# Kernel optimization log

Measured on AMD Instinct MI355X. Metric: run time of the kernel, lower is better.

The kernel has to match this reference:

```python
import jax, jax.numpy as jnp
import numpy as np

H, L, OUT = 128, 3, 128
N, E, NRG, ERG, M, G = 200_000, 600_000, 100_000, 300_000, 200_000, 10_000
BN_EPS = 1e-5


def setup_inputs() -> dict:
    key = jax.random.key(0)
    ks = iter(jax.random.split(key, 32))
    rint = lambda shape, hi: jax.random.randint(next(ks), shape, 0, hi, dtype=jnp.int64 if False else jnp.int32)
    inp = {
        "node_feat": rint((N, 9), 100),
        "edge_index": rint((2, E), N),
        "edge_feat": rint((E, 3), 100),
        "batch": jnp.sort(rint((N,), G)),
        "mapping_row": rint((M,), N),
        "mapping_col": rint((M,), NRG),
        "rg_edge_index": rint((2, ERG), NRG),
        "rg_atom_features": rint((NRG,), 8),
        "tree_batch": jnp.sort(rint((NRG,), G)),
        "num_graphs": G,
    }
    s = 0.05
    nrm = lambda shape: jax.random.normal(next(ks), shape, dtype=jnp.float32) * s
    inp.update({
        "atom_emb": nrm((9, 100, H)),
        "bond_emb": nrm((L, 3, 100, H)),
        "rg_emb": nrm((8, H)),
        "atom_W1": nrm((L, H, 2 * H)),
        "atom_W2": nrm((L, 2 * H, H)),
        "rg_W1": nrm((L, H, 2 * H)),
        "rg_W2": nrm((L, 2 * H, H)),
        "raw2rg_W": nrm((L, H, H)),
        "rg2raw_W": nrm((L, H, H)),
        "atom_lin_W": nrm((H, H)),
        "rg_lin_W": nrm((H, H)),
        "lin_W": nrm((H, OUT)),
    })
    return inp


def _scatter_mean(src, idx, n):
    s = jax.ops.segment_sum(src, idx, num_segments=n)
    c = jax.ops.segment_sum(jnp.ones((src.shape[0], 1), src.dtype), idx, num_segments=n)
    return s / jnp.maximum(c, 1.0)


def _bn(h):  # BatchNorm1d(affine=False), batch statistics
    mu = h.mean(0)
    var = h.var(0)
    return (h - mu) * jax.lax.rsqrt(var + BN_EPS)


def _gin_mlp(h, W1, W2):  # Linear -> BN -> ReLU -> Linear (all bias-free)
    return jax.nn.relu(_bn(h @ W1)) @ W2


def reference(node_feat, edge_index, edge_feat, batch, mapping_row, mapping_col,
              rg_edge_index, rg_atom_features, tree_batch, num_graphs,
              atom_emb, bond_emb, rg_emb, atom_W1, atom_W2, rg_W1, rg_W2,
              raw2rg_W, rg2raw_W, atom_lin_W, rg_lin_W, lin_W):
    n = node_feat.shape[0]
    n_rg = rg_atom_features.shape[0]
    src, dst = edge_index[0], edge_index[1]
    rsrc, rdst = rg_edge_index[0], rg_edge_index[1]

    # AtomEncoder: sum of 9 embedding lookups -> [n, H]
    x = atom_emb[jnp.arange(9), node_feat].sum(axis=1)
    rg = rg_emb[rg_atom_features]  # [n_rg, H]

    for i in range(L):
        # BondEncoder + GINEConv: sum_j relu(x_j + e_ij) aggregated at dst
        e = bond_emb[i][jnp.arange(3), edge_feat].sum(axis=1)  # [E, H]
        agg = jax.ops.segment_sum(jax.nn.relu(x[src] + e), dst, num_segments=n)
        x = jax.nn.relu(_bn(_gin_mlp(x + agg, atom_W1[i], atom_W2[i])))

        # raw -> reduced-graph inter message passing (scatter mean over mapping)
        rg = rg + jax.nn.relu(_scatter_mean(x[mapping_row], mapping_col, n_rg) @ raw2rg_W[i])

        # GINConv on reduced graph
        agg_rg = jax.ops.segment_sum(rg[rsrc], rdst, num_segments=n_rg)
        rg = jax.nn.relu(_bn(_gin_mlp(rg + agg_rg, rg_W1[i], rg_W2[i])))

        # reduced-graph -> raw inter message passing
        x = x + jax.nn.relu(_scatter_mean(rg[mapping_col], mapping_row, n) @ rg2raw_W[i])

    # graph-level readout (mean pooling)
    xg = _scatter_mean(x, batch, num_graphs) @ atom_lin_W
    rgg = _scatter_mean(rg, tree_batch, num_graphs) @ rg_lin_W
    return jax.nn.relu(xg + rgg) @ lin_W  # [num_graphs, OUT]
```

## Files before the change

### kernel.cpp

```cpp
#include <hip/hip_runtime.h>
#include <hip/hip_bf16.h>
#include <cstdint>
#include <cstddef>

#define H 128

using f32x4v = __attribute__((ext_vector_type(4))) float;
using bf8 = __attribute__((ext_vector_type(8))) short;

__device__ __forceinline__ short f2bf(float f) {
  unsigned u = __float_as_uint(f);
  u = (u + 0x7fffu + ((u >> 16) & 1u)) >> 16;
  return (short)u;
}
__device__ __forceinline__ float bf2f(short h) {
  return __uint_as_float(((unsigned)(unsigned short)h) << 16);
}
__device__ __forceinline__ void splitf(float f, short& h, short& l) {
  h = f2bf(f);
  l = f2bf(f - bf2f(h));
}
__device__ __forceinline__ f32x4v mfma16(bf8 a, bf8 b, f32x4v c) {
  return __builtin_amdgcn_mfma_f32_16x16x32_bf16(a, b, c, 0, 0, 0);
}

__device__ __forceinline__ void stage16(const void* gsrc, void* ldst) {
  __builtin_amdgcn_global_load_lds(
      (const __attribute__((address_space(1))) void*)gsrc,
      (__attribute__((address_space(3))) void*)ldst, 16, 0, 0);
}

__device__ __forceinline__ void load_afrags(const float* __restrict__ Ap, bool av,
    float sc, bf8* ah, bf8* al_) {
#pragma unroll
  for (int ks = 0; ks < 4; ++ks) {
    float v[8];
    if (av) {
      f32x4v p0 = *(const f32x4v*)(Ap + ks * 32);
      f32x4v p1 = *(const f32x4v*)(Ap + ks * 32 + 4);
      v[0]=p0.x*sc; v[1]=p0.y*sc; v[2]=p0.z*sc; v[3]=p0.w*sc;
      v[4]=p1.x*sc; v[5]=p1.y*sc; v[6]=p1.z*sc; v[7]=p1.w*sc;
    } else {
#pragma unroll
      for (int j = 0; j < 8; ++j) v[j] = 0.f;
    }
#pragma unroll
    for (int j = 0; j < 8; ++j) { short hh, ll; splitf(v[j], hh, ll); ah[ks][j]=hh; al_[ks][j]=ll; }
  }
}


__global__ __launch_bounds__(256) void pack_w_k(const float* __restrict__ W,
    short* __restrict__ hi, short* __restrict__ lo, int K, int N) {
  int total = K * N;
  int t = blockIdx.x * 256 + threadIdx.x;
  int layer = blockIdx.y;
  if (t >= total) return;
  int k = t / N, n = t - k * N;
  float f = W[(size_t)layer * total + t];
  short h, l; splitf(f, h, l);
  int nt = n >> 4, ks = k >> 5, kk = k & 31;
  int lane = (n & 15) | (((kk >> 3) & 3) << 4);
  size_t idx = (size_t)layer * total + ((size_t)(nt * (K >> 5) + ks) << 9) + lane * 8 + (kk & 7);
  hi[idx] = h; lo[idx] = l;
}


__global__ __launch_bounds__(256) void atom_encode_k(const int* __restrict__ nf,
    const float* __restrict__ emb, float* __restrict__ x, int N) {
  long long t = (long long)blockIdx.x * 256 + threadIdx.x;
  if (t >= (long long)N * H) return;
  int n = (int)(t >> 7), h = (int)(t & 127);
  const int* row = nf + (size_t)n * 9;
  float s = 0.f;
#pragma unroll
  for (int f = 0; f < 9; ++f) s += emb[((size_t)f * 100 + row[f]) * H + h];
  x[t] = s;
}

__global__ __launch_bounds__(256) void rg_init_k(const int* __restrict__ feat,
    const float* __restrict__ emb, float* __restrict__ rg, int NRG) {
  long long t = (long long)blockIdx.x * 256 + threadIdx.x;
  if (t >= (long long)NRG * H) return;
  int n = (int)(t >> 7), h = (int)(t & 127);
  rg[t] = emb[(size_t)feat[n] * H + h];
}


__global__ __launch_bounds__(256) void icount_k(const int* __restrict__ idx,
    int* __restrict__ cnt, int n) {
  int t = blockIdx.x * 256 + threadIdx.x;
  if (t < n) atomicAdd(&cnt[idx[t]], 1);
}

__global__ __launch_bounds__(256) void inv_from_int_k(const int* __restrict__ c,
    float* __restrict__ inv, int n) {
  int t = blockIdx.x * 256 + threadIdx.x;
  if (t < n) inv[t] = 1.0f / (float)max(c[t], 1);
}

__global__ __launch_bounds__(256) void seg_blocksum_k(const int* __restrict__ cnt,
    int* __restrict__ bsum, int n) {
  __shared__ int red[256];
  int base = blockIdx.x * 1024;
  int s = 0;
  for (int i = threadIdx.x; i < 1024; i += 256) {
    int idx = base + i;
    s += (idx < n) ? cnt[idx] : 0;
  }
  red[threadIdx.x] = s; __syncthreads();
  for (int st = 128; st > 0; st >>= 1) {
    if (threadIdx.x < st) red[threadIdx.x] += red[threadIdx.x + st];
    __syncthreads();
  }
  if (threadIdx.x == 0) bsum[blockIdx.x] = red[0];
}

__global__ __launch_bounds__(256) void seg_scan_k(const int* __restrict__ cnt,
    const int* __restrict__ bsum, int* __restrict__ off, int* __restrict__ cur,
    int n, int nblk) {
  __shared__ int pref;
  __shared__ int tsum[257];
  int b = blockIdx.x;
  if (threadIdx.x == 0) {
    int p = 0;
    for (int j = 0; j < b; ++j) p += bsum[j];
    pref = p;
  }
  int base = b * 1024 + threadIdx.x * 4;
  int v[4]; int s = 0;
#pragma unroll
  for (int j = 0; j < 4; ++j) { int idx = base + j; v[j] = (idx < n) ? cnt[idx] : 0; s += v[j]; }
  tsum[threadIdx.x + 1] = s;
  if (threadIdx.x == 0) tsum[0] = 0;
  __syncthreads();
  if (threadIdx.x == 0) { for (int j = 1; j <= 256; ++j) tsum[j] += tsum[j - 1]; }
  __syncthreads();
  int run = pref + tsum[threadIdx.x];
#pragma unroll
  for (int j = 0; j < 4; ++j) {
    int idx = base + j;
    if (idx < n) { off[idx] = run; cur[idx] = run; }
    run += v[j];
  }
  if (b == 0 && threadIdx.x == 0) {
    int tot = 0;
    for (int j = 0; j < nblk; ++j) tot += bsum[j];
    off[n] = tot;
  }
}

__global__ __launch_bounds__(256) void seg_fill_k(const int* __restrict__ idx,
    int* __restrict__ cur, int* __restrict__ ids, int n) {
  int t = blockIdx.x * 256 + threadIdx.x;
  if (t < n) { int p = atomicAdd(&cur[idx[t]], 1); ids[p] = t; }
}


__global__ __launch_bounds__(256) void gine_agg_k(const int* __restrict__ off,
    const int* __restrict__ ids, const int* __restrict__ ei, const int* __restrict__ ef,
    const float* __restrict__ bemb, const float* __restrict__ x,
    float* __restrict__ out, int N) {
  int n = blockIdx.x * 8 + (threadIdx.x >> 5);
  if (n >= N) return;
  int c4 = (threadIdx.x & 31) * 4;
  float4 acc = *(const float4*)(x + (size_t)n * H + c4);
  float4 acc2 = make_float4(0.f, 0.f, 0.f, 0.f);
  int p0 = off[n], p1 = off[n + 1];
  int p = p0;
  for (; p + 1 < p1; p += 2) {
    int e0 = ids[p], e1 = ids[p + 1];
    int s0 = ei[e0], s1 = ei[e1];
    const int* f0 = ef + (size_t)e0 * 3;
    const int* f1 = ef + (size_t)e1 * 3;
    float4 a0 = *(const float4*)(bemb + (size_t)f0[0] * H + c4);
    float4 a1 = *(const float4*)(bemb + ((size_t)100 + f0[1]) * H + c4);
    float4 a2 = *(const float4*)(bemb + ((size_t)200 + f0[2]) * H + c4);
    float4 xa = *(const float4*)(x + (size_t)s0 * H + c4);
    float4 b0 = *(const float4*)(bemb + (size_t)f1[0] * H + c4);
    float4 b1 = *(const float4*)(bemb + ((size_t)100 + f1[1]) * H + c4);
    float4 b2 = *(const float4*)(bemb + ((size_t)200 + f1[2]) * H + c4);
    float4 xb = *(const float4*)(x + (size_t)s1 * H + c4);
    acc.x += fmaxf(xa.x + a0.x + a1.x + a2.x, 0.f);
    acc.y += fmaxf(xa.y + a0.y + a1.y + a2.y, 0.f);
    acc.z += fmaxf(xa.z + a0.z + a1.z + a2.z, 0.f);
    acc.w += fmaxf(xa.w + a0.w + a1.w + a2.w, 0.f);
    acc2.x += fmaxf(xb.x + b0.x + b1.x + b2.x, 0.f);
    acc2.y += fmaxf(xb.y + b0.y + b1.y + b2.y, 0.f);
    acc2.z += fmaxf(xb.z + b0.z + b1.z + b2.z, 0.f);
    acc2.w += fmaxf(xb.w + b0.w + b1.w + b2.w, 0.f);
  }
  if (p < p1) {
    int e = ids[p];
    int src = ei[e];
    const int* f = ef + (size_t)e * 3;
    float4 v0 = *(const float4*)(bemb + (size_t)f[0] * H + c4);
    float4 v1 = *(const float4*)(bemb + ((size_t)100 + f[1]) * H + c4);
    float4 v2 = *(const float4*)(bemb + ((size_t)200 + f[2]) * H + c4);
    float4 xs = *(const float4*)(x + (size_t)src * H + c4);
    acc.x += fmaxf(xs.x + v0.x + v1.x + v2.x, 0.f);
    acc.y += fmaxf(xs.y + v0.y + v1.y + v2.y, 0.f);
    acc.z += fmaxf(xs.z + v0.z + v1.z + v2.z, 0.f);
    acc.w += fmaxf(xs.w + v0.w + v1.w + v2.w, 0.f);
  }
  acc.x += acc2.x; acc.y += acc2.y; acc.z += acc2.z; acc.w += acc2.w;
  *(float4*)(out + (size_t)n * H + c4) = acc;
}

__global__ __launch_bounds__(256) void gather_agg_k(const int* __restrict__ off,
    const int* __restrict__ ids, const int* __restrict__ sidx,
    const float* __restrict__ src, const float* __restrict__ base,
    float* __restrict__ out, int N) {
  int n = blockIdx.x * 8 + (threadIdx.x >> 5);
  if (n >= N) return;
  int c4 = (threadIdx.x & 31) * 4;
  float4 acc = make_float4(0.f, 0.f, 0.f, 0.f);
  float4 acc2 = make_float4(0.f, 0.f, 0.f, 0.f);
  if (base) acc = *(const float4*)(base + (size_t)n * H + c4);
  int p0 = off[n], p1 = off[n + 1];
  int p = p0;
  for (; p + 1 < p1; p += 2) {
    int m0 = ids[p], m1 = ids[p + 1];
    int s0 = sidx ? sidx[m0] : m0;
    int s1 = sidx ? sidx[m1] : m1;
    float4 v0 = *(const float4*)(src + (size_t)s0 * H + c4);
    float4 v1 = *(const float4*)(src + (size_t)s1 * H + c4);
    acc.x += v0.x; acc.y += v0.y; acc.z += v0.z; acc.w += v0.w;
    acc2.x += v1.x; acc2.y += v1.y; acc2.z += v1.z; acc2.w += v1.w;
  }
  if (p < p1) {
    int m = ids[p];
    int sr = sidx ? sidx[m] : m;
    float4 v = *(const float4*)(src + (size_t)sr * H + c4);
    acc.x += v.x; acc.y += v.y; acc.z += v.z; acc.w += v.w;
  }
  acc.x += acc2.x; acc.y += acc2.y; acc.z += acc2.z; acc.w += acc2.w;
  *(float4*)(out + (size_t)n * H + c4) = acc;
}

__device__ __forceinline__ int lowb(const int* __restrict__ a, int n, int v) {
  int lo = 0, hi = n;
  while (lo < hi) { int mid = (lo + hi) >> 1; if (a[mid] < v) lo = mid + 1; else hi = mid; }
  return lo;
}

__global__ __launch_bounds__(256) void pool_mean_k(const int* __restrict__ bidx,
    const float* __restrict__ src, float* __restrict__ out, int n, int G) {
  int g = blockIdx.x * 8 + (threadIdx.x >> 5);
  if (g >= G) return;
  int c4 = (threadIdx.x & 31) * 4;
  int lo = lowb(bidx, n, g), hi = lowb(bidx, n, g + 1);
  float4 acc = make_float4(0.f, 0.f, 0.f, 0.f);
  for (int r = lo; r < hi; ++r) {
    float4 v = *(const float4*)(src + (size_t)r * H + c4);
    acc.x += v.x; acc.y += v.y; acc.z += v.z; acc.w += v.w;
  }
  float inv = 1.0f / (float)max(hi - lo, 1);
  acc.x *= inv; acc.y *= inv; acc.z *= inv; acc.w *= inv;
  *(float4*)(out + (size_t)g * H + c4) = acc;
}


__global__ void bn_final_k(float* __restrict__ ssum, float* __restrict__ ssq,
    float* __restrict__ mu, float* __restrict__ rsig, int C, float invM) {
  int c = threadIdx.x;
  if (c < C) {
    float m = ssum[c] * invM;
    float v = ssq[c] * invM - m * m;
    mu[c] = m;
    rsig[c] = rsqrtf(v + 1e-5f);
  }
  ssum[c] = 0.f;
  ssq[c] = 0.f;
}

__global__ __launch_bounds__(256) void bn_apply_relu_k(const float* __restrict__ X,
    const float* __restrict__ mu, const float* __restrict__ rsig,
    float* __restrict__ Out, int M) {
  long long t = (long long)blockIdx.x * 256 + threadIdx.x;
  if (t >= (long long)M * 32) return;
  int c4 = ((int)(t & 31)) * 4;
  float4 v = ((const float4*)X)[t];
  float4 m4 = *(const float4*)&mu[c4];
  float4 r4 = *(const float4*)&rsig[c4];
  v.x = fmaxf((v.x - m4.x) * r4.x, 0.f);
  v.y = fmaxf((v.y - m4.y) * r4.y, 0.f);
  v.z = fmaxf((v.z - m4.z) * r4.z, 0.f);
  v.w = fmaxf((v.w - m4.w) * r4.w, 0.f);
  ((float4*)Out)[t] = v;
}


__global__ __launch_bounds__(512) void mlp_stats_mfma_k(
    const float* __restrict__ A, const short* __restrict__ w1h, const short* __restrict__ w1l,
    float* __restrict__ ssum, float* __restrict__ ssq, int M, int npairs) {
  __shared__ __align__(16) short Wch[8192], Wcl[8192];
  __shared__ float sRed[256], qRed[256];
  int tid = threadIdx.x;
  if (tid < 256) { sRed[tid] = 0.f; qRed[tid] = 0.f; }
  int w = tid >> 6, l = tid & 63, l15 = l & 15, lg = l >> 4;
  int h = w >> 2, wl = w & 3;
  float sAcc[16], qAcc[16];
#pragma unroll
  for (int nt = 0; nt < 16; ++nt) { sAcc[nt] = 0.f; qAcc[nt] = 0.f; }
  for (int pb = blockIdx.x; pb < npairs; pb += gridDim.x) {
    int tile = pb * 2 + h;
    int arow = tile * 64 + wl * 16 + l15;
    bool av = arow < M;
    bf8 ah[4], al_[4];
    load_afrags(A + (size_t)arow * 128 + lg * 8, av, 1.f, ah, al_);
    for (int ch = 0; ch < 4; ++ch) {
      __syncthreads();
      const bf8* srcH = (const bf8*)(w1h + ch * 8192);
      const bf8* srcL = (const bf8*)(w1l + ch * 8192);
      for (int it = tid; it < 1024; it += 512) {
        stage16(srcH + it, ((bf8*)Wch) + it);
        stage16(srcL + it, ((bf8*)Wcl) + it);
      }
      __syncthreads();
#pragma unroll
      for (int ntl = 0; ntl < 4; ++ntl) {
        f32x4v c = {0.f, 0.f, 0.f, 0.f};
#pragma unroll
        for (int ks = 0; ks < 4; ++ks) {
          bf8 bh = *(const bf8*)&Wch[(ntl * 4 + ks) * 512 + l * 8];
          bf8 bl = *(const bf8*)&Wcl[(ntl * 4 + ks) * 512 + l * 8];
          c = mfma16(al_[ks], bh, c);
          c = mfma16(ah[ks], bl, c);
          c = mfma16(ah[ks], bh, c);
        }
        int nt = ch * 4 + ntl;
        if (av) {
          sAcc[nt] += c[0] + c[1] + c[2] + c[3];
          qAcc[nt] += c[0]*c[0] + c[1]*c[1] + c[2]*c[2] + c[3]*c[3];
        }
      }
    }
  }
  __syncthreads();
#pragma unroll
  for (int nt = 0; nt < 16; ++nt) {
    float s = sAcc[nt], q = qAcc[nt];
    s += __shfl_xor(s, 16); s += __shfl_xor(s, 32);
    q += __shfl_xor(q, 16); q += __shfl_xor(q, 32);
    if (l < 16) { atomicAdd(&sRed[nt * 16 + l], s); atomicAdd(&qRed[nt * 16 + l], q); }
  }
  __syncthreads();
  if (tid < 256) { atomicAdd(&ssum[tid], sRed[tid]); atomicAdd(&ssq[tid], qRed[tid]); }
}


__global__ __launch_bounds__(512) void mlp_fused_mfma_k(
    float* __restrict__ A, const short* __restrict__ w1h, const short* __restrict__ w1l,
    const short* __restrict__ w2h, const short* __restrict__ w2l,
    const float* __restrict__ mu, const float* __restrict__ rsig,
    float* __restrict__ ssum, float* __restrict__ ssq, int M, int npairs) {
  __shared__ __align__(16) short Wch[8192], Wcl[8192];
  __shared__ __align__(16) float h1f[2][64][132];
  __shared__ float sRed[128], qRed[128];
  int tid = threadIdx.x;
  if (tid < 128) { sRed[tid] = 0.f; qRed[tid] = 0.f; }
  int w = tid >> 6, l = tid & 63, l15 = l & 15, lg = l >> 4;
  int h = w >> 2, wl = w & 3;
  float sAcc[8], qAcc[8];
#pragma unroll
  for (int nt = 0; nt < 8; ++nt) { sAcc[nt] = 0.f; qAcc[nt] = 0.f; }
  for (int pb = blockIdx.x; pb < npairs; pb += gridDim.x) {
    int tile = pb * 2 + h;
    int arow = tile * 64 + wl * 16 + l15;
    bool av = arow < M;
    f32x4v acc[8];
#pragma unroll
    for (int nt = 0; nt < 8; ++nt) acc[nt] = (f32x4v){0.f, 0.f, 0.f, 0.f};
    bf8 ah[4], al_[4];
    load_afrags(A + (size_t)arow * 128 + lg * 8, av, 1.f, ah, al_);
    for (int kh = 0; kh < 2; ++kh) {
      {
        for (int ch = 0; ch < 2; ++ch) {
          int cbase = kh * 8 + ch * 4;
          __syncthreads();
          const bf8* srcH = (const bf8*)(w1h + cbase * 2048);
          const bf8* srcL = (const bf8*)(w1l + cbase * 2048);
          for (int it = tid; it < 1024; it += 512) {
            stage16(srcH + it, ((bf8*)Wch) + it);
            stage16(srcL + it, ((bf8*)Wcl) + it);
          }
          __syncthreads();
#pragma unroll
          for (int ntl = 0; ntl < 4; ++ntl) {
            f32x4v c = {0.f, 0.f, 0.f, 0.f};
#pragma unroll
            for (int ks = 0; ks < 4; ++ks) {
              bf8 bh = *(const bf8*)&Wch[(ntl * 4 + ks) * 512 + l * 8];
              bf8 bl = *(const bf8*)&Wcl[(ntl * 4 + ks) * 512 + l * 8];
              c = mfma16(al_[ks], bh, c);
              c = mfma16(ah[ks], bl, c);
              c = mfma16(ah[ks], bh, c);
            }
            int cn = cbase + ntl;
            int cc = cn * 16 + l15;
            float mm = mu[cc], rs = rsig[cc];
#pragma unroll
            for (int r = 0; r < 4; ++r) {
              float t = fmaxf((c[r] - mm) * rs, 0.f);
              h1f[h][wl * 16 + lg * 4 + r][(cn & 7) * 16 + l15] = t;
            }
          }
        }
      }
      __syncthreads();
      bf8 a2h[4], a2l[4];
#pragma unroll
      for (int ks2 = 0; ks2 < 4; ++ks2) {
        const float* hp = &h1f[h][wl * 16 + l15][ks2 * 32 + lg * 8];
#pragma unroll
        for (int j = 0; j < 8; ++j) {
          short hh, ll; splitf(hp[j], hh, ll);
          a2h[ks2][j] = hh; a2l[ks2][j] = ll;
        }
      }
      for (int c2 = 0; c2 < 2; ++c2) {
        __syncthreads();
        for (int it = tid; it < 1024; it += 512) {
          int e = it * 8;
          int ntl = e >> 11, rem = e & 2047;
          int ks2 = rem >> 9, s = rem & 511;
          int src = ((c2 * 4 + ntl) * 8 + kh * 4 + ks2) * 512 + s;
          stage16((const bf8*)(w2h + src), ((bf8*)Wch) + it);
          stage16((const bf8*)(w2l + src), ((bf8*)Wcl) + it);
        }
        __syncthreads();
#pragma unroll
        for (int ntl = 0; ntl < 4; ++ntl) {
          f32x4v c = acc[c2 * 4 + ntl];
#pragma unroll
          for (int ks2 = 0; ks2 < 4; ++ks2) {
            bf8 bh = *(const bf8*)&Wch[(ntl * 4 + ks2) * 512 + l * 8];
            bf8 bl = *(const bf8*)&Wcl[(ntl * 4 + ks2) * 512 + l * 8];
            c = mfma16(a2l[ks2], bh, c);
            c = mfma16(a2h[ks2], bl, c);
            c = mfma16(a2h[ks2], bh, c);
          }
          acc[c2 * 4 + ntl] = c;
        }
      }
    }
    int base = tile * 64 + wl * 16;
#pragma unroll
    for (int nt = 0; nt < 8; ++nt) {
      int cc = nt * 16 + l15;
#pragma unroll
      for (int r = 0; r < 4; ++r) {
        int gr = base + lg * 4 + r;
        if (gr < M) {
          float vv = acc[nt][r];
          A[(size_t)gr * 128 + cc] = vv;
          sAcc[nt] += vv;
          qAcc[nt] = fmaf(vv, vv, qAcc[nt]);
        }
      }
    }
  }
  __syncthreads();
#pragma unroll
  for (int nt = 0; nt < 8; ++nt) {
    float s = sAcc[nt], q = qAcc[nt];
    s += __shfl_xor(s, 16); s += __shfl_xor(s, 32);
    q += __shfl_xor(q, 16); q += __shfl_xor(q, 32);
    if (l < 16) { atomicAdd(&sRed[nt * 16 + l], s); atomicAdd(&qRed[nt * 16 + l], q); }
  }
  __syncthreads();
  if (tid < 128) { atomicAdd(&ssum[tid], sRed[tid]); atomicAdd(&ssq[tid], qRed[tid]); }
}


__global__ __launch_bounds__(256) void gemm128_mfma_k(
    const float* __restrict__ A0, const float* __restrict__ AUX,
    const short* __restrict__ wh, const short* __restrict__ wl,
    float* __restrict__ Out, int M, int ntiles) {
  __shared__ __align__(16) short Wh[16384];
  int tid = threadIdx.x;
  for (int i = tid; i < 2048; i += 256) {
    stage16((const f32x4v*)wh + i, ((f32x4v*)Wh) + i);
  }
  __syncthreads();
  int w = tid >> 6, l = tid & 63, l15 = l & 15, lg = l >> 4;
  const bf8* wlp = (const bf8*)wl;
  for (int tb = blockIdx.x; tb < ntiles; tb += gridDim.x) {
    int arow = tb * 64 + w * 16 + l15;
    bool av = arow < M;
    float sc = av ? AUX[arow] : 0.f;
    bf8 ah[4], al_[4];
    load_afrags(A0 + (size_t)arow * 128 + lg * 8, av, sc, ah, al_);
    int base = tb * 64 + w * 16;
#pragma unroll 2
    for (int nt = 0; nt < 8; ++nt) {
      f32x4v c = {0.f, 0.f, 0.f, 0.f};
#pragma unroll
      for (int ks = 0; ks < 4; ++ks) {
        bf8 bh = *(const bf8*)&Wh[(nt * 4 + ks) * 512 + l * 8];
        bf8 bl = wlp[(nt * 4 + ks) * 64 + l];
        c = mfma16(al_[ks], bh, c);
        c = mfma16(ah[ks], bl, c);
        c = mfma16(ah[ks], bh, c);
      }
#pragma unroll
      for (int r = 0; r < 4; ++r) {
        int gr = base + lg * 4 + r;
        if (gr < M) {
          size_t o = (size_t)gr * 128 + nt * 16 + l15;
          Out[o] = Out[o] + fmaxf(c[r], 0.f);
        }
      }
    }
  }
}

template<int EPI>
__global__ __launch_bounds__(256) void gemm_k(
    const float* __restrict__ A0, const float* __restrict__ W,
    float* __restrict__ Out, int M) {
  __shared__ __align__(16) float Ash[64][64];
  int tid = threadIdx.x;
  int tc = tid & 63, tr = tid >> 6;
  int row0 = blockIdx.x * 64;
  float acc[16][2];
#pragma unroll
  for (int i = 0; i < 16; ++i) { acc[i][0] = 0.f; acc[i][1] = 0.f; }
  for (int k0 = 0; k0 < 128; k0 += 64) {
#pragma unroll
    for (int it = 0; it < 4; ++it) {
      int fidx = tid + it * 256;
      int r = fidx >> 4, c4 = (fidx & 15) << 2;
      int gr = row0 + r;
      float4 v = make_float4(0.f, 0.f, 0.f, 0.f);
      if (gr < M) v = *(const float4*)(A0 + (size_t)gr * 128 + k0 + c4);
      *(float4*)&Ash[r][c4] = v;
    }
    __syncthreads();
    const float* Wp = W + (size_t)k0 * 128 + tc;
    for (int kk = 0; kk < 64; kk += 4) {
      float w[4][2];
#pragma unroll
      for (int kj = 0; kj < 4; ++kj)
#pragma unroll
        for (int j = 0; j < 2; ++j) w[kj][j] = Wp[(size_t)(kk + kj) * 128 + j * 64];
#pragma unroll
      for (int i = 0; i < 16; ++i) {
        float4 a = *(const float4*)&Ash[tr * 16 + i][kk];
#pragma unroll
        for (int j = 0; j < 2; ++j) {
          acc[i][j] = fmaf(a.x, w[0][j], acc[i][j]);
          acc[i][j] = fmaf(a.y, w[1][j], acc[i][j]);
          acc[i][j] = fmaf(a.z, w[2][j], acc[i][j]);
          acc[i][j] = fmaf(a.w, w[3][j], acc[i][j]);
        }
      }
    }
    __syncthreads();
  }
#pragma unroll
  for (int i = 0; i < 16; ++i) {
    int gr = row0 + tr * 16 + i;
    if (gr < M) {
#pragma unroll
      for (int j = 0; j < 2; ++j) {
        size_t o = (size_t)gr * 128 + tc + j * 64;
        float v = acc[i][j];
        if (EPI == 0) Out[o] = v;
        else Out[o] = fmaxf(Out[o] + v, 0.f);
      }
    }
  }
}


static inline int cdivll(long long a, long long b) { return (int)((a + b - 1) / b); }

extern "C" void kernel_launch(void* const* d_in, const int* in_sizes, int n_in,
                              void* d_out, int out_size, void* d_ws, size_t ws_size,
                              hipStream_t stream) {
  const int* node_feat  = (const int*)d_in[0];
  const int* edge_index = (const int*)d_in[1];
  const int* edge_feat  = (const int*)d_in[2];
  const int* batch      = (const int*)d_in[3];
  const int* map_row    = (const int*)d_in[4];
  const int* map_col    = (const int*)d_in[5];
  const int* rg_ei      = (const int*)d_in[6];
  const int* rg_feat    = (const int*)d_in[7];
  const int* tree_batch = (const int*)d_in[8];
  const float* atom_emb   = (const float*)d_in[10];
  const float* bond_emb   = (const float*)d_in[11];
  const float* rg_emb     = (const float*)d_in[12];
  const float* atom_W1    = (const float*)d_in[13];
  const float* atom_W2    = (const float*)d_in[14];
  const float* rg_W1      = (const float*)d_in[15];
  const float* rg_W2      = (const float*)d_in[16];
  const float* raw2rg_W   = (const float*)d_in[17];
  const float* rg2raw_W   = (const float*)d_in[18];
  const float* atom_lin_W = (const float*)d_in[19];
  const float* rg_lin_W   = (const float*)d_in[20];
  const float* lin_W      = (const float*)d_in[21];

  const int N   = in_sizes[0] / 9;
  const int E   = in_sizes[1] / 2;
  const int M   = in_sizes[4];
  const int NRG = in_sizes[7];
  const int ERG = in_sizes[6] / 2;
  const int G   = out_size / H;
  if (N <= 0 || G <= 0) return;

  const size_t NH = (size_t)N * H, RH = (size_t)NRG * H, GH = (size_t)G * H;
  const int cmax = max(N, NRG);

  const size_t nfloat = 2 * NH + RH + (size_t)NRG + (size_t)N + 2048;
  const size_t nint = (size_t)(N + 1) * 2 + (size_t)(NRG + 1) * 2
                    + (size_t)E + 2 * (size_t)M + (size_t)ERG + (size_t)cmax + 1024;
  const size_t nshort = 3 * (4 * 32768 + 2 * 16384);
  const size_t need = nfloat * 4 + nint * 4 + nshort * 2 + 256;
  if (ws_size < need) return;

  float* ws = (float*)d_ws;
  size_t off = 0;
  auto alloc = [&](size_t n) { float* p = ws + off; off += n; return p; };
  float* x       = alloc(NH);
  float* abuf    = alloc(NH);
  float* rg      = alloc(RH);
  float* inv_col = alloc((size_t)NRG);
  float* inv_row = alloc((size_t)N);
  float* ssum = alloc(256);
  float* ssq  = alloc(256);
  float* mu   = alloc(256);
  float* rsig = alloc(256);

  int* ip = (int*)(ws + off);
  size_t ioff = 0;
  auto ialloc = [&](size_t n) { int* p = ip + ioff; ioff += n; return p; };
  int* off_dst = ialloc((size_t)N + 1);
  int* off_col = ialloc((size_t)NRG + 1);
  int* off_row = ialloc((size_t)N + 1);
  int* off_rg  = ialloc((size_t)NRG + 1);
  int* ids_dst = ialloc((size_t)E);
  int* ids_col = ialloc((size_t)M);
  int* ids_row = ialloc((size_t)M);
  int* ids_rg  = ialloc((size_t)ERG);
  int* tmp_cnt = ialloc((size_t)cmax);
  int* bsum    = ialloc(1024);

  short* sp = (short*)(ip + ioff);
  size_t soff = 0;
  auto salloc = [&](size_t n) { short* p = sp + soff; soff += n; return p; };
  short* paW1h = salloc(3 * 32768); short* paW1l = salloc(3 * 32768);
  short* paW2h = salloc(3 * 32768); short* paW2l = salloc(3 * 32768);
  short* prW1h = salloc(3 * 32768); short* prW1l = salloc(3 * 32768);
  short* prW2h = salloc(3 * 32768); short* prW2l = salloc(3 * 32768);
  short* p2gh  = salloc(3 * 16384); short* p2gl  = salloc(3 * 16384);
  short* pg2h  = salloc(3 * 16384); short* pg2l  = salloc(3 * 16384);

  const int ta = (N + 63) >> 6, trg = (NRG + 63) >> 6;
  const int pa = (ta + 1) >> 1, prg = (trg + 1) >> 1;
  const int ga2 = pa < 512 ? pa : 512, grg2 = prg < 512 ? prg : 512;
  const int ga = ta < 1024 ? ta : 1024, grg = trg < 1024 ? trg : 1024;

  pack_w_k<<<dim3(128, 3), 256, 0, stream>>>(atom_W1, paW1h, paW1l, 128, 256);
  pack_w_k<<<dim3(128, 3), 256, 0, stream>>>(atom_W2, paW2h, paW2l, 256, 128);
  pack_w_k<<<dim3(128, 3), 256, 0, stream>>>(rg_W1, prW1h, prW1l, 128, 256);
  pack_w_k<<<dim3(128, 3), 256, 0, stream>>>(rg_W2, prW2h, prW2l, 256, 128);
  pack_w_k<<<dim3(64, 3), 256, 0, stream>>>(raw2rg_W, p2gh, p2gl, 128, 128);
  pack_w_k<<<dim3(64, 3), 256, 0, stream>>>(rg2raw_W, pg2h, pg2l, 128, 128);

  auto build_csr = [&](const int* idx, int nelem, int nrows, int* offs, int* ids,
                       float* inv) {
    hipMemsetAsync(tmp_cnt, 0, (size_t)nrows * 4, stream);
    icount_k<<<cdivll(nelem, 256), 256, 0, stream>>>(idx, tmp_cnt, nelem);
    if (inv) inv_from_int_k<<<cdivll(nrows, 256), 256, 0, stream>>>(tmp_cnt, inv, nrows);
    int nblk = cdivll(nrows, 1024);
    seg_blocksum_k<<<nblk, 256, 0, stream>>>(tmp_cnt, bsum, nrows);
    seg_scan_k<<<nblk, 256, 0, stream>>>(tmp_cnt, bsum, offs, tmp_cnt, nrows, nblk);
    seg_fill_k<<<cdivll(nelem, 256), 256, 0, stream>>>(idx, tmp_cnt, ids, nelem);
  };
  build_csr(edge_index + E, E, N, off_dst, ids_dst, nullptr);
  build_csr(map_col, M, NRG, off_col, ids_col, inv_col);
  build_csr(map_row, M, N, off_row, ids_row, inv_row);
  build_csr(rg_ei + ERG, ERG, NRG, off_rg, ids_rg, nullptr);

  hipMemsetAsync(ssum, 0, 512 * 4, stream);
  atom_encode_k<<<cdivll(NH, 256), 256, 0, stream>>>(node_feat, atom_emb, x, N);
  rg_init_k<<<cdivll(RH, 256), 256, 0, stream>>>(rg_feat, rg_emb, rg, NRG);

  for (int i = 0; i < 3; ++i) {
    gine_agg_k<<<cdivll(N, 8), 256, 0, stream>>>(off_dst, ids_dst, edge_index, edge_feat,
        bond_emb + (size_t)i * 3 * 100 * H, x, abuf, N);
    mlp_stats_mfma_k<<<ga2, 512, 0, stream>>>(abuf, paW1h + i * 32768, paW1l + i * 32768, ssum, ssq, N, pa);
    bn_final_k<<<1, 256, 0, stream>>>(ssum, ssq, mu, rsig, 256, 1.0f / N);
    mlp_fused_mfma_k<<<ga2, 512, 0, stream>>>(abuf, paW1h + i * 32768, paW1l + i * 32768,
        paW2h + i * 32768, paW2l + i * 32768, mu, rsig, ssum, ssq, N, pa);
    bn_final_k<<<1, 256, 0, stream>>>(ssum, ssq, mu, rsig, 128, 1.0f / N);
    bn_apply_relu_k<<<cdivll((long long)N * 32, 256), 256, 0, stream>>>(abuf, mu, rsig, x, N);

    gather_agg_k<<<cdivll(NRG, 8), 256, 0, stream>>>(off_col, ids_col, map_row, x, nullptr, abuf, NRG);
    gemm128_mfma_k<<<grg, 256, 0, stream>>>(abuf, inv_col, p2gh + i * 16384, p2gl + i * 16384,
        rg, NRG, trg);

    gather_agg_k<<<cdivll(NRG, 8), 256, 0, stream>>>(off_rg, ids_rg, rg_ei, rg, rg, abuf, NRG);
    mlp_stats_mfma_k<<<grg2, 512, 0, stream>>>(abuf, prW1h + i * 32768, prW1l + i * 32768, ssum, ssq, NRG, prg);
    bn_final_k<<<1, 256, 0, stream>>>(ssum, ssq, mu, rsig, 256, 1.0f / NRG);
    mlp_fused_mfma_k<<<grg2, 512, 0, stream>>>(abuf, prW1h + i * 32768, prW1l + i * 32768,
        prW2h + i * 32768, prW2l + i * 32768, mu, rsig, ssum, ssq, NRG, prg);
    bn_final_k<<<1, 256, 0, stream>>>(ssum, ssq, mu, rsig, 128, 1.0f / NRG);
    bn_apply_relu_k<<<cdivll((long long)NRG * 32, 256), 256, 0, stream>>>(abuf, mu, rsig, rg, NRG);

    gather_agg_k<<<cdivll(N, 8), 256, 0, stream>>>(off_row, ids_row, map_col, rg, nullptr, abuf, N);
    gemm128_mfma_k<<<ga, 256, 0, stream>>>(abuf, inv_row, pg2h + i * 16384, pg2l + i * 16384,
        x, N, ta);
  }

  float* xg  = abuf;
  float* rgg = abuf + GH;
  float* P   = abuf + 2 * GH;
  pool_mean_k<<<cdivll(G, 8), 256, 0, stream>>>(batch, x, xg, N, G);
  pool_mean_k<<<cdivll(G, 8), 256, 0, stream>>>(tree_batch, rg, rgg, NRG, G);
  gemm_k<0><<<cdivll(G, 64), 256, 0, stream>>>(xg, atom_lin_W, P, G);
  gemm_k<2><<<cdivll(G, 64), 256, 0, stream>>>(rgg, rg_lin_W, P, G);
  gemm_k<0><<<cdivll(G, 64), 256, 0, stream>>>(P, lin_W, (float*)d_out, G);
}
```

Before: 2.635 ms.

## Double-buffer weight chunks in LDS to overlap staging with MFMA in fused MLP

Result: no change. 2.593 ms, median of 2 (-1.6%).

```diff
diff --git a/kernel.cpp b/kernel.cpp
--- a/kernel.cpp
+++ b/kernel.cpp
@@ -355,7 +355,7 @@
     const short* __restrict__ w2h, const short* __restrict__ w2l,
     const float* __restrict__ mu, const float* __restrict__ rsig,
     float* __restrict__ ssum, float* __restrict__ ssq, int M, int npairs) {
-  __shared__ __align__(16) short Wch[8192], Wcl[8192];
+  __shared__ __align__(16) short Wch[2][8192], Wcl[2][8192];
   __shared__ __align__(16) float h1f[2][64][132];
   __shared__ float sRed[128], qRed[128];
   int tid = threadIdx.x;
@@ -374,42 +374,49 @@
     for (int nt = 0; nt < 8; ++nt) acc[nt] = (f32x4v){0.f, 0.f, 0.f, 0.f};
     bf8 ah[4], al_[4];
     load_afrags(A + (size_t)arow * 128 + lg * 8, av, 1.f, ah, al_);
-    for (int kh = 0; kh < 2; ++kh) {
-      {
-        for (int ch = 0; ch < 2; ++ch) {
-          int cbase = kh * 8 + ch * 4;
-          __syncthreads();
-          const bf8* srcH = (const bf8*)(w1h + cbase * 2048);
-          const bf8* srcL = (const bf8*)(w1l + cbase * 2048);
-          for (int it = tid; it < 1024; it += 512) {
-            stage16(srcH + it, ((bf8*)Wch) + it);
-            stage16(srcL + it, ((bf8*)Wcl) + it);
-          }
-          __syncthreads();
-#pragma unroll
-          for (int ntl = 0; ntl < 4; ++ntl) {
-            f32x4v c = {0.f, 0.f, 0.f, 0.f};
-#pragma unroll
-            for (int ks = 0; ks < 4; ++ks) {
-              bf8 bh = *(const bf8*)&Wch[(ntl * 4 + ks) * 512 + l * 8];
-              bf8 bl = *(const bf8*)&Wcl[(ntl * 4 + ks) * 512 + l * 8];
-              c = mfma16(al_[ks], bh, c);
-              c = mfma16(ah[ks], bl, c);
-              c = mfma16(ah[ks], bh, c);
-            }
-            int cn = cbase + ntl;
-            int cc = cn * 16 + l15;
-            float mm = mu[cc], rs = rsig[cc];
-#pragma unroll
-            for (int r = 0; r < 4; ++r) {
-              float t = fmaxf((c[r] - mm) * rs, 0.f);
-              h1f[h][wl * 16 + lg * 4 + r][(cn & 7) * 16 + l15] = t;
-            }
-          }
-        }
-      }
-      __syncthreads();
-      bf8 a2h[4], a2l[4];
+    bf8 a2h[4], a2l[4];
+
+    auto stageW1 = [&](int cbase, int buf) {
+      const bf8* srcH = (const bf8*)(w1h + cbase * 2048);
+      const bf8* srcL = (const bf8*)(w1l + cbase * 2048);
+      for (int it = tid; it < 1024; it += 512) {
+        stage16(srcH + it, ((bf8*)Wch[buf]) + it);
+        stage16(srcL + it, ((bf8*)Wcl[buf]) + it);
+      }
+    };
+    auto stageW2 = [&](int kh, int c2, int buf) {
+      for (int it = tid; it < 1024; it += 512) {
+        int e = it * 8;
+        int ntl = e >> 11, rem = e & 2047;
+        int ks2 = rem >> 9, s = rem & 511;
+        int src = ((c2 * 4 + ntl) * 8 + kh * 4 + ks2) * 512 + s;
+        stage16((const bf8*)(w2h + src), ((bf8*)Wch[buf]) + it);
+        stage16((const bf8*)(w2l + src), ((bf8*)Wcl[buf]) + it);
+      }
+    };
+    auto mfmaW1 = [&](int cbase, int buf) {
+#pragma unroll
+      for (int ntl = 0; ntl < 4; ++ntl) {
+        f32x4v c = {0.f, 0.f, 0.f, 0.f};
+#pragma unroll
+        for (int ks = 0; ks < 4; ++ks) {
+          bf8 bh = *(const bf8*)&Wch[buf][(ntl * 4 + ks) * 512 + l * 8];
+          bf8 bl = *(const bf8*)&Wcl[buf][(ntl * 4 + ks) * 512 + l * 8];
+          c = mfma16(al_[ks], bh, c);
+          c = mfma16(ah[ks], bl, c);
+          c = mfma16(ah[ks], bh, c);
+        }
+        int cn = cbase + ntl;
+        int cc = cn * 16 + l15;
+        float mm = mu[cc], rs = rsig[cc];
+#pragma unroll
+        for (int r = 0; r < 4; ++r) {
+          float t = fmaxf((c[r] - mm) * rs, 0.f);
+          h1f[h][wl * 16 + lg * 4 + r][(cn & 7) * 16 + l15] = t;
+        }
+      }
+    };
+    auto buildA2 = [&]() {
 #pragma unroll
       for (int ks2 = 0; ks2 < 4; ++ks2) {
         const float* hp = &h1f[h][wl * 16 + l15][ks2 * 32 + lg * 8];
@@ -419,32 +426,51 @@
           a2h[ks2][j] = hh; a2l[ks2][j] = ll;
         }
       }
-      for (int c2 = 0; c2 < 2; ++c2) {
-        __syncthreads();
-        for (int it = tid; it < 1024; it += 512) {
-          int e = it * 8;
-          int ntl = e >> 11, rem = e & 2047;
-          int ks2 = rem >> 9, s = rem & 511;
-          int src = ((c2 * 4 + ntl) * 8 + kh * 4 + ks2) * 512 + s;
-          stage16((const bf8*)(w2h + src), ((bf8*)Wch) + it);
-          stage16((const bf8*)(w2l + src), ((bf8*)Wcl) + it);
-        }
-        __syncthreads();
-#pragma unroll
-        for (int ntl = 0; ntl < 4; ++ntl) {
-          f32x4v c = acc[c2 * 4 + ntl];
-#pragma unroll
-          for (int ks2 = 0; ks2 < 4; ++ks2) {
-            bf8 bh = *(const bf8*)&Wch[(ntl * 4 + ks2) * 512 + l * 8];
-            bf8 bl = *(const bf8*)&Wcl[(ntl * 4 + ks2) * 512 + l * 8];
-            c = mfma16(a2l[ks2], bh, c);
-            c = mfma16(a2h[ks2], bl, c);
-            c = mfma16(a2h[ks2], bh, c);
-          }
-          acc[c2 * 4 + ntl] = c;
-        }
-      }
-    }
+    };
+    auto mfmaW2 = [&](int c2, int buf) {
+#pragma unroll
+      for (int ntl = 0; ntl < 4; ++ntl) {
+        f32x4v c = acc[c2 * 4 + ntl];
+#pragma unroll
+        for (int ks2 = 0; ks2 < 4; ++ks2) {
+          bf8 bh = *(const bf8*)&Wch[buf][(ntl * 4 + ks2) * 512 + l * 8];
+          bf8 bl = *(const bf8*)&Wcl[buf][(ntl * 4 + ks2) * 512 + l * 8];
+          c = mfma16(a2l[ks2], bh, c);
+          c = mfma16(a2h[ks2], bl, c);
+          c = mfma16(a2h[ks2], bh, c);
+        }
+        acc[c2 * 4 + ntl] = c;
+      }
+    };
+
+    __syncthreads();
+    stageW1(0, 0);
+    __syncthreads();
+    stageW1(4, 1);
+    mfmaW1(0, 0);
+    __syncthreads();
+    stageW2(0, 0, 0);
+    mfmaW1(4, 1);
+    buildA2();
+    __syncthreads();
+    stageW2(0, 1, 1);
+    mfmaW2(0, 0);
+    __syncthreads();
+    stageW1(8, 0);
+    mfmaW2(1, 1);
+    __syncthreads();
+    stageW1(12, 1);
+    mfmaW1(8, 0);
+    __syncthreads();
+    stageW2(1, 0, 0);
+    mfmaW1(12, 1);
+    buildA2();
+    __syncthreads();
+    stageW2(1, 1, 1);
+    mfmaW2(0, 0);
+    __syncthreads();
+    mfmaW2(1, 1);
+
     int base = tile * 64 + wl * 16;
 #pragma unroll
     for (int nt = 0; nt < 8; ++nt) {
```
